# Performance work log

Measured on AMD Instinct MI355X. Metric: run time of the kernel, lower is better.

Reference implementation:

```python
import jax, jax.numpy as jnp
import numpy as np

INPUT_SIZE = 2
HIDDEN = 128
OUTPUT = 2
FUTURE = 50


def setup_inputs() -> dict:
    key = jax.random.key(0)
    ks = jax.random.split(key, 7)
    B, T = 4096, 512
    s = 1.0 / np.sqrt(HIDDEN)
    x = jax.random.normal(ks[0], (B, T, INPUT_SIZE), dtype=jnp.float32)
    W_ih = jax.random.uniform(ks[1], (4 * HIDDEN, INPUT_SIZE), minval=-s, maxval=s, dtype=jnp.float32)
    W_hh = jax.random.uniform(ks[2], (4 * HIDDEN, HIDDEN), minval=-s, maxval=s, dtype=jnp.float32)
    b_ih = jax.random.uniform(ks[3], (4 * HIDDEN,), minval=-s, maxval=s, dtype=jnp.float32)
    b_hh = jax.random.uniform(ks[4], (4 * HIDDEN,), minval=-s, maxval=s, dtype=jnp.float32)
    fc_w = jax.random.uniform(ks[5], (OUTPUT, HIDDEN), minval=-s, maxval=s, dtype=jnp.float32)
    fc_b = jax.random.uniform(ks[6], (OUTPUT,), minval=-s, maxval=s, dtype=jnp.float32)
    return {"x": x, "W_ih": W_ih, "W_hh": W_hh, "b_ih": b_ih, "b_hh": b_hh, "fc_w": fc_w, "fc_b": fc_b}


def reference(x, W_ih, W_hh, b_ih, b_hh, fc_w, fc_b):
    B = x.shape[0]

    def cell(h, c, xt):
        # gates: [B, 4H], PyTorch LSTMCell order i, f, g, o
        gates = xt @ W_ih.T + b_ih + h @ W_hh.T + b_hh
        i, f, g, o = jnp.split(gates, 4, axis=-1)
        c_new = jax.nn.sigmoid(f) * c + jax.nn.sigmoid(i) * jnp.tanh(g)
        h_new = jax.nn.sigmoid(o) * jnp.tanh(c_new)
        return h_new, c_new

    h0 = jnp.zeros((B, HIDDEN), dtype=x.dtype)
    c0 = jnp.zeros((B, HIDDEN), dtype=x.dtype)

    def encode_step(carry, xt):
        h, c = carry
        h, c = cell(h, c, xt)
        return (h, c), None

    (h, c), _ = jax.lax.scan(encode_step, (h0, c0), jnp.swapaxes(x, 0, 1))

    def forecast_step(carry, _):
        h, c = carry
        y = h @ fc_w.T + fc_b  # [B, OUTPUT]
        h, c = cell(h, c, y)
        return (h, c), y

    (_, _), ys = jax.lax.scan(forecast_step, (h, c), None, length=FUTURE)
    # ys: [FUTURE, B, OUTPUT] -> torch.cat(outputs, dim=1) -> [B, FUTURE*OUTPUT]
    return jnp.swapaxes(ys, 0, 1).reshape(B, FUTURE * OUTPUT)
```

## Files before the change

kernel.cpp:

```cpp
#include <hip/hip_runtime.h>

#define HIDDEN 128
#define TSTEPS 512
#define NFUT 50
#define BR 16
#define THREADS 512
#define HPITCH 136

typedef __bf16 bf16x8 __attribute__((ext_vector_type(8)));
typedef float floatx4 __attribute__((ext_vector_type(4)));
typedef float f32x2 __attribute__((ext_vector_type(2)));

union B8 { int4 i; bf16x8 v; };

#if defined(__has_builtin)
#  if __has_builtin(__builtin_amdgcn_exp2f)
#    define EXP2F(x) __builtin_amdgcn_exp2f(x)
#  else
#    define EXP2F(x) exp2f(x)
#  endif
#  if __has_builtin(__builtin_amdgcn_rcpf)
#    define RCPF(x) __builtin_amdgcn_rcpf(x)
#  else
#    define RCPF(x) (1.0f / (x))
#  endif
#  if __has_builtin(__builtin_amdgcn_s_setprio)
#    define SETPRIO(p) __builtin_amdgcn_s_setprio(p)
#  else
#    define SETPRIO(p)
#  endif
#else
#  define EXP2F(x) exp2f(x)
#  define RCPF(x) (1.0f / (x))
#  define SETPRIO(p)
#endif

#define L2E  1.4426950408889634f
#define L2E2 2.8853900817779268f

__global__ __launch_bounds__(THREADS, 2)
void lstm_forecast_kernel(const float* __restrict__ x,
                          const float* __restrict__ W_ih,
                          const float* __restrict__ W_hh,
                          const float* __restrict__ b_ih,
                          const float* __restrict__ b_hh,
                          const float* __restrict__ fc_w,
                          const float* __restrict__ fc_b,
                          float* __restrict__ out) {
    __shared__ __align__(16) uint2  xa[TSTEPS * BR];
    __shared__ __align__(16) __bf16 h_lds[2][BR * HPITCH];
    __shared__ __align__(16) float  fcw_lds[2][HIDDEN];

    const int tid  = threadIdx.x;
    const int wave = tid >> 6;
    const int lane = tid & 63;
    const int quad = lane >> 4;
    const int l15  = lane & 15;
    const int rb   = blockIdx.x * BR;

    if (tid < 256) fcw_lds[tid >> 7][tid & 127] = fc_w[tid];

    {
        const int row = tid & 15;
        for (int tb = tid >> 4; tb < TSTEPS; tb += THREADS >> 4) {
            float2 xv = *(const float2*)&x[(size_t)(rb + row) * (2 * TSTEPS) + tb * 2];
            __bf16 x0h = (__bf16)xv.x, x1h = (__bf16)xv.y;
            __bf16 x0r = (__bf16)(xv.x - (float)x0h);
            __bf16 x1r = (__bf16)(xv.y - (float)x1h);
            uint2 d;
            d.x = (unsigned)__builtin_bit_cast(unsigned short, x0h) |
                  ((unsigned)__builtin_bit_cast(unsigned short, x1h) << 16);
            d.y = (unsigned)__builtin_bit_cast(unsigned short, x0r) |
                  ((unsigned)__builtin_bit_cast(unsigned short, x1r) << 16);
            xa[tb * BR + row] = d;
        }
    }
    for (int i = tid; i < BR * HPITCH; i += THREADS) h_lds[0][i] = (__bf16)0.0f;

    bf16x8 bfrag[4][4];
    B8 bfx[4];
    float gs[4];
    const float fcb0 = fc_b[0], fcb1 = fc_b[1];
    const int ub    = wave * 16 + l15;
    const int cbase = wave * 16 + quad * 4;
#pragma unroll
    for (int g = 0; g < 4; ++g) {
        gs[g] = (g == 2) ? -L2E2 : -L2E;
        const int cg = g * HIDDEN + ub;
        const float w0 = W_ih[cg * 2 + 0];
        const float w1 = W_ih[cg * 2 + 1];
        const float bs = b_ih[cg] + b_hh[cg];
#pragma unroll
        for (int ks = 0; ks < 4; ++ks) {
            const float* wp = W_hh + (size_t)cg * HIDDEN + ks * 32 + quad * 8;
            bf16x8 bb;
#pragma unroll
            for (int j = 0; j < 8; ++j) bb[j] = (__bf16)(gs[g] * wp[j]);
            bfrag[g][ks] = bb;
        }
        B8 t; t.i = make_int4(0, 0, 0, 0);
        if (quad == 0) {
            const float w0s = gs[g] * w0, w1s = gs[g] * w1, bss = gs[g] * bs;
            __bf16 w0h = (__bf16)w0s, w1h = (__bf16)w1s;
            __bf16 w0l = (__bf16)(w0s - (float)w0h);
            __bf16 w1l = (__bf16)(w1s - (float)w1h);
            __bf16 bh  = (__bf16)bss;
            __bf16 bl  = (__bf16)(bss - (float)bh);
            bf16x8 bv = {w0h, w1h, bh, bl, w0h, w1h, w0l, w1l};
            t.v = bv;
        }
        bfx[g] = t;
    }

    const unsigned ones2 = 0x3F803F80u;
    const int hrow = l15 * HPITCH;
    f32x2 cst[2] = {{0.f, 0.f}, {0.f, 0.f}};

    auto pk2 = [](f32x2 hn) -> unsigned {
        return (unsigned)__builtin_bit_cast(unsigned short, (__bf16)hn.x)
             | ((unsigned)__builtin_bit_cast(unsigned short, (__bf16)hn.y) << 16);
    };

    auto ewTail = [&](floatx4 a0, floatx4 a1, floatx4 a2, floatx4 a3, __bf16* hd) {
        floatx4 ea, ec, eb, eo;
#pragma unroll
        for (int r = 0; r < 4; ++r) ea[r] = EXP2F(a0[r]);
#pragma unroll
        for (int r = 0; r < 4; ++r) ec[r] = EXP2F(a1[r]);
#pragma unroll
        for (int r = 0; r < 4; ++r) eb[r] = EXP2F(a2[r]);
#pragma unroll
        for (int r = 0; r < 4; ++r) eo[r] = EXP2F(a3[r]);
        unsigned wArr[2];
#pragma unroll
        for (int p = 0; p < 2; ++p) {
            const f32x2 eap = {ea[2 * p], ea[2 * p + 1]};
            const f32x2 ebp = {eb[2 * p], eb[2 * p + 1]};
            const f32x2 ecp = {ec[2 * p], ec[2 * p + 1]};
            const f32x2 eop = {eo[2 * p], eo[2 * p + 1]};
            const f32x2 A1 = 1.f + eap, B1 = 1.f + ebp, C1 = 1.f + ecp;
            const f32x2 P  = A1 * B1;
            const f32x2 PC = P * C1;
            f32x2 R;
            { const float I = RCPF(PC.x * PC.y); R.x = I * PC.y; R.y = I * PC.x; }
            const f32x2 sfv = P * R;
            const f32x2 igv = (1.f - ebp) * (C1 * R);
            const f32x2 cn  = sfv * cst[p] + igv;
            cst[p] = cn;
            const f32x2 am = -L2E2 * cn;
            f32x2 ed;
            ed.x = EXP2F(fminf(am.x, 29.f));
            ed.y = EXP2F(fminf(am.y, 29.f));
            const f32x2 E = (1.f + ed) * (1.f + eop);
            f32x2 R2;
            { const float J = RCPF(E.x * E.y); R2.x = J * E.y; R2.y = J * E.x; }
            const f32x2 hn = (1.f - ed) * R2;
            wArr[p] = pk2(hn);
        }
        uint2 wv; wv.x = wArr[0]; wv.y = wArr[1];
        *(uint2*)&hd[hrow + cbase] = wv;
    };

    auto cellE = [&](const __bf16* hs, __bf16* hd, uint2 xd, int tn) -> uint2 {
        B8 xf; xf.i = make_int4((int)xd.x, (int)ones2, (int)xd.y, (int)xd.x);
        bf16x8 af[4];
#pragma unroll
        for (int ks = 0; ks < 4; ++ks)
            af[ks] = *(const bf16x8*)&hs[hrow + ks * 32 + quad * 8];
        const floatx4 z = {0.f, 0.f, 0.f, 0.f};
        floatx4 acc[4];
        SETPRIO(1);
#pragma unroll
        for (int g = 0; g < 4; ++g)
            acc[g] = __builtin_amdgcn_mfma_f32_16x16x32_bf16(bfx[g].v, xf.v, z, 0, 0, 0);
#pragma unroll
        for (int ks = 0; ks < 4; ++ks)
#pragma unroll
            for (int g = 0; g < 4; ++g)
                acc[g] = __builtin_amdgcn_mfma_f32_16x16x32_bf16(bfrag[g][ks], af[ks], acc[g], 0, 0, 0);
        SETPRIO(0);
        const int ts = (tn < TSTEPS) ? tn : 0;
        const uint2 xn = xa[ts * BR + l15];
        ewTail(acc[0], acc[1], acc[2], acc[3], hd);
        __syncthreads();
        return xn;
    };

    __syncthreads();

    uint2 xd = xa[l15];
    for (int t = 0; t < TSTEPS; t += 2) {
        xd = cellE(h_lds[0], h_lds[1], xd, t + 1);
        xd = cellE(h_lds[1], h_lds[0], xd, t + 2);
    }

    floatx4 beff[4];
#pragma unroll
    for (int g = 0; g < 4; ++g) {
        const int cgA = g * HIDDEN + ub;
        const float wi0 = W_ih[cgA * 2 + 0];
        const float wi1 = W_ih[cgA * 2 + 1];
#pragma unroll
        for (int ks = 0; ks < 4; ++ks) {
            const int k0 = ks * 32 + quad * 8;
            bf16x8 bb = bfrag[g][ks];
#pragma unroll
            for (int j = 0; j < 8; ++j)
                bb[j] = (__bf16)((float)bb[j] + gs[g] * (wi0 * fcw_lds[0][k0 + j]
                                                       + wi1 * fcw_lds[1][k0 + j]));
            bfrag[g][ks] = bb;
        }
        floatx4 v;
#pragma unroll
        for (int r = 0; r < 4; ++r) {
            const int cg = g * HIDDEN + cbase + r;
            v[r] = gs[g] * (b_ih[cg] + b_hh[cg]
                          + W_ih[cg * 2 + 0] * fcb0 + W_ih[cg * 2 + 1] * fcb1);
        }
        beff[g] = v;
    }

    auto cellF = [&](const __bf16* hs, __bf16* hd) {
        bf16x8 af[4];
#pragma unroll
        for (int ks = 0; ks < 4; ++ks)
            af[ks] = *(const bf16x8*)&hs[hrow + ks * 32 + quad * 8];
        floatx4 acc[4];
#pragma unroll
        for (int g = 0; g < 4; ++g) acc[g] = beff[g];
        SETPRIO(1);
#pragma unroll
        for (int ks = 0; ks < 4; ++ks)
#pragma unroll
            for (int g = 0; g < 4; ++g)
                acc[g] = __builtin_amdgcn_mfma_f32_16x16x32_bf16(bfrag[g][ks], af[ks], acc[g], 0, 0, 0);
        SETPRIO(0);
        ewTail(acc[0], acc[1], acc[2], acc[3], hd);
        __syncthreads();
    };

    auto emitY = [&](const __bf16* hs, int f) {
        if (wave == 0) {
            const int r = lane & 15, seg = lane >> 4;
            const __bf16* hp = &hs[r * HPITCH + seg * 32];
            float p0 = 0.f, p1 = 0.f;
#pragma unroll
            for (int js = 0; js < 4; ++js) {
                bf16x8 hv = *(const bf16x8*)&hp[js * 8];
                const float4* f0 = (const float4*)&fcw_lds[0][seg * 32 + js * 8];
                const float4* f1 = (const float4*)&fcw_lds[1][seg * 32 + js * 8];
                float4 a0 = f0[0], b0 = f0[1], a1 = f1[0], b1 = f1[1];
                p0 += (float)hv[0]*a0.x + (float)hv[1]*a0.y + (float)hv[2]*a0.z + (float)hv[3]*a0.w
                    + (float)hv[4]*b0.x + (float)hv[5]*b0.y + (float)hv[6]*b0.z + (float)hv[7]*b0.w;
                p1 += (float)hv[0]*a1.x + (float)hv[1]*a1.y + (float)hv[2]*a1.z + (float)hv[3]*a1.w
                    + (float)hv[4]*b1.x + (float)hv[5]*b1.y + (float)hv[6]*b1.z + (float)hv[7]*b1.w;
            }
            p0 += __shfl_xor(p0, 16); p0 += __shfl_xor(p0, 32);
            p1 += __shfl_xor(p1, 16); p1 += __shfl_xor(p1, 32);
            if (seg == 0) {
                float* op = &out[(size_t)(rb + r) * (2 * NFUT) + f * 2];
                op[0] = p0 + fcb0;
                op[1] = p1 + fcb1;
            }
        }
    };

    for (int f = 0; f < NFUT; f += 2) {
        emitY(h_lds[0], f);
        cellF(h_lds[0], h_lds[1]);
        emitY(h_lds[1], f + 1);
        cellF(h_lds[1], h_lds[0]);
    }
}

extern "C" void kernel_launch(void* const* d_in, const int* in_sizes, int n_in,
                              void* d_out, int out_size, void* d_ws, size_t ws_size,
                              hipStream_t stream) {
    const float* x    = (const float*)d_in[0];
    const float* W_ih = (const float*)d_in[1];
    const float* W_hh = (const float*)d_in[2];
    const float* b_ih = (const float*)d_in[3];
    const float* b_hh = (const float*)d_in[4];
    const float* fc_w = (const float*)d_in[5];
    const float* fc_b = (const float*)d_in[6];
    float* out = (float*)d_out;

    const int B = in_sizes[0] / (TSTEPS * 2);
    const int grid = B / BR;
    lstm_forecast_kernel<<<grid, THREADS, 0, stream>>>(x, W_ih, W_hh, b_ih, b_hh, fc_w, fc_b, out);
}
```

Baseline: 477.6 us.

## Halve batch rows per block and split elementwise work across half-waves

Each block now handles 8 batch rows instead of 16, which doubles the grid. The MFMA still computes 16 columns, so the padding rows 8-15 read zeros from LDS. The elementwise LSTM tail now uses lane shuffles so that each lane processes two gate outputs instead of four, and launch bounds request 4 blocks per CU. This aims for more blocks in flight and a shorter serial elementwise tail per step, at the cost of wasting half of every MFMA and adding shuffle overhead.

Result: slower. 801.2 us (+67.8%).

```diff
diff --git a/kernel.cpp b/kernel.cpp
--- a/kernel.cpp
+++ b/kernel.cpp
@@ -3,7 +3,7 @@
 #define HIDDEN 128
 #define TSTEPS 512
 #define NFUT 50
-#define BR 16
+#define BR 8
 #define THREADS 512
 #define HPITCH 136
 
@@ -38,7 +38,7 @@
 #define L2E  1.4426950408889634f
 #define L2E2 2.8853900817779268f
 
-__global__ __launch_bounds__(THREADS, 2)
+__global__ __launch_bounds__(THREADS, 4)
 void lstm_forecast_kernel(const float* __restrict__ x,
                           const float* __restrict__ W_ih,
                           const float* __restrict__ W_hh,
@@ -48,7 +48,7 @@
                           const float* __restrict__ fc_b,
                           float* __restrict__ out) {
     __shared__ __align__(16) uint2  xa[TSTEPS * BR];
-    __shared__ __align__(16) __bf16 h_lds[2][BR * HPITCH];
+    __shared__ __align__(16) __bf16 h_lds[2][16 * HPITCH];
     __shared__ __align__(16) float  fcw_lds[2][HIDDEN];
 
     const int tid  = threadIdx.x;
@@ -56,13 +56,15 @@
     const int lane = tid & 63;
     const int quad = lane >> 4;
     const int l15  = lane & 15;
+    const int hi8  = (lane >> 3) & 1;
+    const int row8 = lane & 7;
     const int rb   = blockIdx.x * BR;
 
     if (tid < 256) fcw_lds[tid >> 7][tid & 127] = fc_w[tid];
 
     {
-        const int row = tid & 15;
-        for (int tb = tid >> 4; tb < TSTEPS; tb += THREADS >> 4) {
+        const int row = tid & 7;
+        for (int tb = tid >> 3; tb < TSTEPS; tb += THREADS >> 3) {
             float2 xv = *(const float2*)&x[(size_t)(rb + row) * (2 * TSTEPS) + tb * 2];
             __bf16 x0h = (__bf16)xv.x, x1h = (__bf16)xv.y;
             __bf16 x0r = (__bf16)(xv.x - (float)x0h);
@@ -75,7 +77,7 @@
             xa[tb * BR + row] = d;
         }
     }
-    for (int i = tid; i < BR * HPITCH; i += THREADS) h_lds[0][i] = (__bf16)0.0f;
+    for (int i = tid; i < 2 * 16 * HPITCH; i += THREADS) (&h_lds[0][0])[i] = (__bf16)0.0f;
 
     bf16x8 bfrag[4][4];
     B8 bfx[4];
@@ -114,51 +116,53 @@
 
     const unsigned ones2 = 0x3F803F80u;
     const int hrow = l15 * HPITCH;
-    f32x2 cst[2] = {{0.f, 0.f}, {0.f, 0.f}};
-
+    f32x2 cst = {0.f, 0.f};
+
+    auto mk = [](float a, float b) { f32x2 r; r.x = a; r.y = b; return r; };
     auto pk2 = [](f32x2 hn) -> unsigned {
         return (unsigned)__builtin_bit_cast(unsigned short, (__bf16)hn.x)
              | ((unsigned)__builtin_bit_cast(unsigned short, (__bf16)hn.y) << 16);
     };
 
-    auto ewTail = [&](floatx4 a0, floatx4 a1, floatx4 a2, floatx4 a3, __bf16* hd) {
-        floatx4 ea, ec, eb, eo;
-#pragma unroll
-        for (int r = 0; r < 4; ++r) ea[r] = EXP2F(a0[r]);
-#pragma unroll
-        for (int r = 0; r < 4; ++r) ec[r] = EXP2F(a1[r]);
-#pragma unroll
-        for (int r = 0; r < 4; ++r) eb[r] = EXP2F(a2[r]);
-#pragma unroll
-        for (int r = 0; r < 4; ++r) eo[r] = EXP2F(a3[r]);
-        unsigned wArr[2];
-#pragma unroll
-        for (int p = 0; p < 2; ++p) {
-            const f32x2 eap = {ea[2 * p], ea[2 * p + 1]};
-            const f32x2 ebp = {eb[2 * p], eb[2 * p + 1]};
-            const f32x2 ecp = {ec[2 * p], ec[2 * p + 1]};
-            const f32x2 eop = {eo[2 * p], eo[2 * p + 1]};
-            const f32x2 A1 = 1.f + eap, B1 = 1.f + ebp, C1 = 1.f + ecp;
-            const f32x2 P  = A1 * B1;
-            const f32x2 PC = P * C1;
-            f32x2 R;
-            { const float I = RCPF(PC.x * PC.y); R.x = I * PC.y; R.y = I * PC.x; }
-            const f32x2 sfv = P * R;
-            const f32x2 igv = (1.f - ebp) * (C1 * R);
-            const f32x2 cn  = sfv * cst[p] + igv;
-            cst[p] = cn;
-            const f32x2 am = -L2E2 * cn;
-            f32x2 ed;
-            ed.x = EXP2F(fminf(am.x, 29.f));
-            ed.y = EXP2F(fminf(am.y, 29.f));
-            const f32x2 E = (1.f + ed) * (1.f + eop);
-            f32x2 R2;
-            { const float J = RCPF(E.x * E.y); R2.x = J * E.y; R2.y = J * E.x; }
-            const f32x2 hn = (1.f - ed) * R2;
-            wArr[p] = pk2(hn);
-        }
-        uint2 wv; wv.x = wArr[0]; wv.y = wArr[1];
-        *(uint2*)&hd[hrow + cbase] = wv;
+    auto ewPair = [&](f32x2 gi, f32x2 gf, f32x2 gg, f32x2 go) -> unsigned {
+        f32x2 ea, ec, eb, eo;
+        ea.x = EXP2F(gi.x); ea.y = EXP2F(gi.y);
+        ec.x = EXP2F(gf.x); ec.y = EXP2F(gf.y);
+        eb.x = EXP2F(gg.x); eb.y = EXP2F(gg.y);
+        eo.x = EXP2F(go.x); eo.y = EXP2F(go.y);
+        const f32x2 A1 = 1.f + ea, B1 = 1.f + eb, C1 = 1.f + ec;
+        const f32x2 P  = A1 * B1;
+        const f32x2 PC = P * C1;
+        f32x2 R;
+        { const float I = RCPF(PC.x * PC.y); R.x = I * PC.y; R.y = I * PC.x; }
+        const f32x2 sfv = P * R;
+        const f32x2 igv = (1.f - eb) * (C1 * R);
+        const f32x2 cn  = sfv * cst + igv;
+        cst = cn;
+        const f32x2 am = -L2E2 * cn;
+        f32x2 ed;
+        ed.x = EXP2F(fminf(am.x, 29.f));
+        ed.y = EXP2F(fminf(am.y, 29.f));
+        const f32x2 E = (1.f + ed) * (1.f + eo);
+        f32x2 R2;
+        { const float J = RCPF(E.x * E.y); R2.x = J * E.y; R2.y = J * E.x; }
+        const f32x2 hn = (1.f - ed) * R2;
+        return pk2(hn);
+    };
+
+    auto finish = [&](floatx4 a0, floatx4 a1, floatx4 a2, floatx4 a3, __bf16* hd) {
+        const int src = lane & ~8;
+        float s2[4], s3[4];
+        s2[0] = __shfl(a0[2], src); s3[0] = __shfl(a0[3], src);
+        s2[1] = __shfl(a1[2], src); s3[1] = __shfl(a1[3], src);
+        s2[2] = __shfl(a2[2], src); s3[2] = __shfl(a2[3], src);
+        s2[3] = __shfl(a3[2], src); s3[3] = __shfl(a3[3], src);
+        const f32x2 gi = hi8 ? mk(s2[0], s3[0]) : mk(a0[0], a0[1]);
+        const f32x2 gf = hi8 ? mk(s2[1], s3[1]) : mk(a1[0], a1[1]);
+        const f32x2 gg = hi8 ? mk(s2[2], s3[2]) : mk(a2[0], a2[1]);
+        const f32x2 go = hi8 ? mk(s2[3], s3[3]) : mk(a3[0], a3[1]);
+        const unsigned pkd = ewPair(gi, gf, gg, go);
+        *(unsigned*)&hd[row8 * HPITCH + cbase + hi8 * 2] = pkd;
     };
 
     auto cellE = [&](const __bf16* hs, __bf16* hd, uint2 xd, int tn) -> uint2 {
@@ -180,15 +184,15 @@
                 acc[g] = __builtin_amdgcn_mfma_f32_16x16x32_bf16(bfrag[g][ks], af[ks], acc[g], 0, 0, 0);
         SETPRIO(0);
         const int ts = (tn < TSTEPS) ? tn : 0;
-        const uint2 xn = xa[ts * BR + l15];
-        ewTail(acc[0], acc[1], acc[2], acc[3], hd);
+        const uint2 xn = xa[ts * BR + row8];
+        finish(acc[0], acc[1], acc[2], acc[3], hd);
         __syncthreads();
         return xn;
     };
 
     __syncthreads();
 
-    uint2 xd = xa[l15];
+    uint2 xd = xa[row8];
     for (int t = 0; t < TSTEPS; t += 2) {
         xd = cellE(h_lds[0], h_lds[1], xd, t + 1);
         xd = cellE(h_lds[1], h_lds[0], xd, t + 2);
@@ -235,28 +239,28 @@
             for (int g = 0; g < 4; ++g)
                 acc[g] = __builtin_amdgcn_mfma_f32_16x16x32_bf16(bfrag[g][ks], af[ks], acc[g], 0, 0, 0);
         SETPRIO(0);
-        ewTail(acc[0], acc[1], acc[2], acc[3], hd);
+        finish(acc[0], acc[1], acc[2], acc[3], hd);
         __syncthreads();
     };
 
     auto emitY = [&](const __bf16* hs, int f) {
         if (wave == 0) {
-            const int r = lane & 15, seg = lane >> 4;
-            const __bf16* hp = &hs[r * HPITCH + seg * 32];
+            const int r = lane & 7, seg = lane >> 3;
+            const __bf16* hp = &hs[r * HPITCH + seg * 16];
             float p0 = 0.f, p1 = 0.f;
 #pragma unroll
-            for (int js = 0; js < 4; ++js) {
+            for (int js = 0; js < 2; ++js) {
                 bf16x8 hv = *(const bf16x8*)&hp[js * 8];
-                const float4* f0 = (const float4*)&fcw_lds[0][seg * 32 + js * 8];
-                const float4* f1 = (const float4*)&fcw_lds[1][seg * 32 + js * 8];
+                const float4* f0 = (const float4*)&fcw_lds[0][seg * 16 + js * 8];
+                const float4* f1 = (const float4*)&fcw_lds[1][seg * 16 + js * 8];
                 float4 a0 = f0[0], b0 = f0[1], a1 = f1[0], b1 = f1[1];
                 p0 += (float)hv[0]*a0.x + (float)hv[1]*a0.y + (float)hv[2]*a0.z + (float)hv[3]*a0.w
                     + (float)hv[4]*b0.x + (float)hv[5]*b0.y + (float)hv[6]*b0.z + (float)hv[7]*b0.w;
                 p1 += (float)hv[0]*a1.x + (float)hv[1]*a1.y + (float)hv[2]*a1.z + (float)hv[3]*a1.w
                     + (float)hv[4]*b1.x + (float)hv[5]*b1.y + (float)hv[6]*b1.z + (float)hv[7]*b1.w;
             }
-            p0 += __shfl_xor(p0, 16); p0 += __shfl_xor(p0, 32);
-            p1 += __shfl_xor(p1, 16); p1 += __shfl_xor(p1, 32);
+            p0 += __shfl_xor(p0, 8); p0 += __shfl_xor(p0, 16); p0 += __shfl_xor(p0, 32);
+            p1 += __shfl_xor(p1, 8); p1 += __shfl_xor(p1, 16); p1 += __shfl_xor(p1, 32);
             if (seg == 0) {
                 float* op = &out[(size_t)(rb + r) * (2 * NFUT) + f * 2];
                 op[0] = p0 + fcb0;
```
